# Kernel tuning notes

Hardware: AMD Instinct MI355X
Metric: run time of the kernel (lower is better)

## Reference

```python
import jax, jax.numpy as jnp
import numpy as np

FS = 64      # FIGURE_SEZE
HALF = 32    # FS // 2
STD = 12     # STD_LEN
BATCH = 4    # BATCH_SIZE
EPS = 1e-3   # keras BatchNormalization default epsilon
CC = 256     # cycleCount (multiple of BATCH)
D = FS * HALF  # 2048, dense in/out width


def _split(x):
    # Checkerboard boolean-mask gather: mask[i,j] = ((i + j) % 2 == 0).
    # Row-major flatten of data[mask] -> for even rows take even cols, odd rows odd cols.
    x4 = x.reshape(-1, FS, HALF, 2)                    # [N, FS, HALF, 2]
    par = (jnp.arange(FS) % 2)[None, :, None, None]    # per-row column parity
    u1 = jnp.take_along_axis(x4, par, axis=3)[..., 0]  # masked half   [N, FS, HALF]
    u2 = jnp.take_along_axis(x4, 1 - par, axis=3)[..., 0]  # demasked half
    return u1, u2


def _bn_dense(u, p):
    # computeF/computeG: flatten -> inference BatchNorm -> Dense(2048) -> reshape
    g, be, m, v, W, b = p
    s = u.reshape(u.shape[0], D)
    s = g * (s - m) * jax.lax.rsqrt(v + EPS) + be
    s = s @ W + b
    return s.reshape(-1, FS, HALF)


def _spread(w, off):
    # w @ expandM: place the 32 columns of w at columns off, off+2, ... of a 64-wide zero mat
    z = jnp.zeros((w.shape[0], FS, FS), w.dtype)
    return z.at[:, :, off::2].set(w)


def _move_even(mat, d):
    # keep even rows; roll odd rows along the column axis by d (== tf diag-matmul + roll)
    even = (jnp.arange(FS) % 2 == 0)[:, None]
    return jnp.where(even, mat, jnp.roll(mat, d, axis=2))


def _mix(w1, w2):
    return _move_even(_spread(w1, 0), -1) + _move_even(_spread(w2, 1), 1)


def _encoder(x, F, G):
    u1, u2 = _split(x.reshape(-1, FS, FS))
    v1 = u1 + _bn_dense(u2, F)
    w2 = u2 + _bn_dense(v1, G)
    return _mix(v1, w2).reshape(-1, STD, FS, FS)


def _decoder(y, F, G):
    w1, w2 = _split(y.reshape(-1, FS, FS))
    v2 = w2 - _bn_dense(w1, G)
    u1 = w1 - _bn_dense(v2, F)
    return _mix(u1, v2).reshape(-1, STD, FS, FS)


def _forward(inputs, W1, b1, g1, be1, m1, v1, W3, b3, g3, be3, m3, v3, kop):
    x = inputs                                   # [CC, STD, FS, FS]
    cc = x.shape[0]
    F = (g1, be1, m1, v1, W1, b1)
    G = (g3, be3, m3, v3, W3, b3)
    phiX = _encoder(x, F, G)
    dephiPhiX = _decoder(phiX, F, G)
    # Koopman step: reshape to [BATCH, cc//BATCH, ...], transpose, right-multiply K
    p = phiX.reshape(BATCH, cc // BATCH, STD, FS, FS).transpose(1, 0, 2, 3, 4)
    kPhix = (p @ kop).reshape(-1, STD, FS, FS)
    dePhiKPhiX = _decoder(kPhix, F, G)
    return (x, phiX, dephiPhiX, kPhix, dePhiKPhiX, x[:, 1:], phiX[:, 1:])


def setup_inputs() -> dict:
    key = jax.random.key(0)
    ks = jax.random.split(key, 16)
    inp = {
        "inputs": jax.random.normal(ks[0], (CC, STD, FS, FS), jnp.float32),
        "indexs": jax.random.randint(ks[1], (CC,), 0, 100),  # unused by forward
        "W1": jax.random.normal(ks[2], (D, 2048), jnp.float32) * 0.02,
        "b1": jnp.zeros((2048,), jnp.float32),
        "g1": jax.random.uniform(ks[3], (D,), jnp.float32, 0.9, 1.1),
        "be1": jax.random.normal(ks[4], (D,), jnp.float32) * 0.01,
        "m1": jax.random.normal(ks[5], (D,), jnp.float32) * 0.01,
        "v1": jax.random.uniform(ks[6], (D,), jnp.float32, 0.5, 1.5),
        "W3": jax.random.normal(ks[7], (D, 2048), jnp.float32) * 0.02,
        "b3": jnp.zeros((2048,), jnp.float32),
        "g3": jax.random.uniform(ks[8], (D,), jnp.float32, 0.9, 1.1),
        "be3": jax.random.normal(ks[9], (D,), jnp.float32) * 0.01,
        "m3": jax.random.normal(ks[10], (D,), jnp.float32) * 0.01,
        "v3": jax.random.uniform(ks[11], (D,), jnp.float32, 0.5, 1.5),
        "kop": jax.random.normal(ks[12], (FS, FS), jnp.float32) * 0.125,
    }
    return inp


def reference(inputs, indexs, W1, b1, g1, be1, m1, v1, W3, b3, g3, be3, m3, v3, kop):
    del indexs  # unused in the original call()
    return _forward(inputs, W1, b1, g1, be1, m1, v1, W3, b3, g3, be3, m3, v3, kop)
```

## Files before the change

### kernel.cpp

```cpp
#include <hip/hip_runtime.h>

#define DDIM 2048
#define NROWS 3072

typedef float f32x4 __attribute__((ext_vector_type(4)));
typedef __bf16 bf16x8 __attribute__((ext_vector_type(8)));

__device__ __forceinline__ unsigned short f32_bf16(float f) {
    unsigned int u = __float_as_uint(f);
    u += 0x7fffu + ((u >> 16) & 1u);
    return (unsigned short)(u >> 16);
}

__device__ __forceinline__ void gl2lds16(const unsigned short* g, unsigned short* l) {
    __builtin_amdgcn_global_load_lds(
        (__attribute__((address_space(1))) void*)g,
        (__attribute__((address_space(3))) void*)l, 16, 0, 0);
}

__global__ __launch_bounds__(256) void prep_scal(
    const float* __restrict__ g1, const float* __restrict__ be1,
    const float* __restrict__ m1, const float* __restrict__ v1,
    const float* __restrict__ b1, float* __restrict__ a1, float* __restrict__ c1, float* __restrict__ bp1,
    const float* __restrict__ g3, const float* __restrict__ be3,
    const float* __restrict__ m3, const float* __restrict__ v3,
    const float* __restrict__ b3, float* __restrict__ a3, float* __restrict__ c3, float* __restrict__ bp3)
{
    int n = blockIdx.x * 256 + threadIdx.x;
    if (n < DDIM) {
        float av1 = g1[n] / sqrtf(v1[n] + 1e-3f);
        a1[n] = av1; c1[n] = be1[n] - m1[n] * av1; bp1[n] = b1[n];
        float av3 = g3[n] / sqrtf(v3[n] + 1e-3f);
        a3[n] = av3; c3[n] = be3[n] - m3[n] * av3; bp3[n] = b3[n];
    }
}

__global__ __launch_bounds__(256) void prep_w(
    const float* __restrict__ W, const float* __restrict__ a, unsigned short* __restrict__ Wt)
{
    __shared__ float tile[64][65];
    const int kt = blockIdx.x * 64, nt = blockIdx.y * 64;
    const int t = threadIdx.x;
#pragma unroll
    for (int q = 0; q < 16; ++q) {
        int lin = q * 256 + t;
        int r = lin >> 6, c = lin & 63;
        tile[r][c] = a[kt + r] * W[(size_t)(kt + r) * DDIM + nt + c];
    }
    __syncthreads();
#pragma unroll
    for (int q = 0; q < 16; ++q) {
        int lin = q * 256 + t;
        int r = lin >> 6, c = lin & 63;
        Wt[(size_t)(nt + r) * DDIM + kt + c] = f32_bf16(tile[c][r]);
    }
}

__global__ __launch_bounds__(256) void prep_bpart(
    const float* __restrict__ W, const float* __restrict__ c, float* __restrict__ bp)
{
    int n = blockIdx.x * 256 + threadIdx.x;
    int k0 = blockIdx.y * 128;
    float acc = 0.f;
#pragma unroll 4
    for (int k = k0; k < k0 + 128; ++k) acc += c[k] * W[(size_t)k * DDIM + n];
    atomicAdd(&bp[n], acc);
}

__global__ __launch_bounds__(256) void split_x(
    const float* __restrict__ x, float* __restrict__ o0,
    float* __restrict__ o5, unsigned short* __restrict__ u2b)
{
    int idx = blockIdx.x * 256 + threadIdx.x;
    int n = idx >> 11, rem = idx & 2047, i = rem >> 5, h = rem & 31;
    int base = (n << 12) + (i << 6) + (h << 1);
    float2 xv = *(const float2*)(x + base);
    *(float2*)(o0 + base) = xv;
    int cc = n / 12, s = n - cc * 12;
    if (s >= 1) {
        int tb = ((cc * 11 + (s - 1)) << 12) + (i << 6) + (h << 1);
        *(float2*)(o5 + tb) = xv;
    }
    u2b[idx] = f32_bf16((i & 1) ? xv.x : xv.y);
}

template<bool TAIL>
__global__ __launch_bounds__(256) void mix_k(
    const float* __restrict__ A, const float* __restrict__ B,
    float* __restrict__ Y, float* __restrict__ Yt, unsigned short* __restrict__ Wb)
{
    int idx = blockIdx.x * 256 + threadIdx.x;
    int n = idx >> 11, rem = idx & 2047, i = rem >> 5, h = rem & 31;
    const float* Ar = A + (n << 11) + (i << 5);
    const float* Br = B + (n << 11) + (i << 5);
    float2 yv;
    if ((i & 1) == 0) { yv.x = Ar[h]; yv.y = Br[h]; }
    else             { yv.x = Br[(h + 31) & 31]; yv.y = Ar[(h + 1) & 31]; }
    int base = (n << 12) + (i << 6) + (h << 1);
    *(float2*)(Y + base) = yv;
    if (TAIL) {
        int cc = n / 12, s = n - cc * 12;
        if (s >= 1)
            *(float2*)(Yt + (((cc * 11 + s - 1) << 12) + (i << 6) + (h << 1))) = yv;
        Wb[idx] = f32_bf16((i & 1) ? yv.y : yv.x);
    }
}

__global__ __launch_bounds__(256) void koop_k(
    const float* __restrict__ phiX, const float* __restrict__ kop,
    float* __restrict__ out, unsigned short* __restrict__ Wb)
{
    __shared__ float P[64][65];
    __shared__ alignas(16) float Kp[64][64];
    const int t = threadIdx.x;
    const int np = blockIdx.x;
    int ccp = np / 12, s = np - ccp * 12;
    int src = (((ccp & 3) << 6) + (ccp >> 2)) * 12 + s;
    const float* Ps = phiX + (size_t)src * 4096;
#pragma unroll
    for (int q = 0; q < 16; ++q) {
        int lin = q * 256 + t, r = lin >> 6, c = lin & 63;
        P[r][c] = Ps[lin];
        Kp[r][c] = kop[lin];
    }
    __syncthreads();
    const int jq = (t & 15) << 2;
    const int i0 = (t >> 4) << 2;
    f32x4 acc[4];
#pragma unroll
    for (int r = 0; r < 4; ++r) acc[r] = f32x4{0.f, 0.f, 0.f, 0.f};
    for (int k = 0; k < 64; ++k) {
        f32x4 kv = *(const f32x4*)&Kp[k][jq];
#pragma unroll
        for (int r = 0; r < 4; ++r) acc[r] += P[i0 + r][k] * kv;
    }
    float* o = out + (size_t)np * 4096;
#pragma unroll
    for (int r = 0; r < 4; ++r) {
        const int i = i0 + r;
        *(f32x4*)(o + i * 64 + jq) = acc[r];
        const int par = i & 1;
        unsigned int w0 = f32_bf16(acc[r][par]);
        unsigned int w1v = f32_bf16(acc[r][2 + par]);
        *(unsigned int*)(Wb + (size_t)np * 2048 + i * 32 + (jq >> 1)) = w0 | (w1v << 16);
    }
}

template<int PARX, bool NEG, bool WBF>
__global__ __launch_bounds__(256, 3) void gemm_k(
    const unsigned short* __restrict__ Abf, const unsigned short* __restrict__ Wt,
    const float* __restrict__ bp, const float* __restrict__ resid,
    float* __restrict__ Cf, unsigned short* __restrict__ Cb)
{
    __shared__ alignas(16) unsigned short As[128][64];
    __shared__ alignas(16) unsigned short Bs[128][64];
    const int t = threadIdx.x;
    const int lane = t & 63, wave = t >> 6;
    const int quad = lane >> 4, l16 = lane & 15;
    const int m0 = blockIdx.x * 128;
    const int n0 = blockIdx.y * 128;
    const int wm = (wave >> 1) << 6;
    const int wn = (wave & 1) << 6;

    const int srow = lane >> 3;
    const int cdata = (lane & 7) ^ srow;
    const unsigned short* Ag = Abf + (size_t)(m0 + wave * 32 + srow) * DDIM + (cdata << 3);
    const unsigned short* Bg = Wt  + (size_t)(n0 + wave * 32 + srow) * DDIM + (cdata << 3);
    unsigned short* AslBase = &As[wave * 32][0];
    unsigned short* BslBase = &Bs[wave * 32][0];

    f32x4 acc[4][4];
#pragma unroll
    for (int a = 0; a < 4; ++a)
#pragma unroll
        for (int b = 0; b < 4; ++b) acc[a][b] = f32x4{0.f, 0.f, 0.f, 0.f};

    for (int k0 = 0; k0 < DDIM; k0 += 64) {
        __syncthreads();
#pragma unroll
        for (int j = 0; j < 4; ++j) {
            gl2lds16(Ag + (size_t)(j * 8) * DDIM + k0, AslBase + j * 8 * 64);
            gl2lds16(Bg + (size_t)(j * 8) * DDIM + k0, BslBase + j * 8 * 64);
        }
        __syncthreads();

#pragma unroll
        for (int kk = 0; kk < 2; ++kk) {
            bf16x8 af[4], bfr[4];
#pragma unroll
            for (int mi = 0; mi < 4; ++mi) {
                const int r = wm + mi * 16 + l16;
                af[mi] = *(const bf16x8*)&As[r][(((kk << 2) | quad) ^ (l16 & 7)) << 3];
            }
#pragma unroll
            for (int ni = 0; ni < 4; ++ni) {
                const int r = wn + ni * 16 + l16;
                bfr[ni] = *(const bf16x8*)&Bs[r][(((kk << 2) | quad) ^ (l16 & 7)) << 3];
            }
#pragma unroll
            for (int mi = 0; mi < 4; ++mi)
#pragma unroll
                for (int ni = 0; ni < 4; ++ni)
                    acc[mi][ni] = __builtin_amdgcn_mfma_f32_16x16x32_bf16(
                        af[mi], bfr[ni], acc[mi][ni], 0, 0, 0);
        }
    }

#pragma unroll
    for (int ni = 0; ni < 4; ++ni) {
        const int n = n0 + wn + ni * 16 + l16;
        const float bias = bp[n];
        const int i = n >> 5, h = n & 31;
        const int par = (i & 1) ^ PARX;
#pragma unroll
        for (int mi = 0; mi < 4; ++mi) {
            const int mbase = m0 + wm + mi * 16 + (quad << 2);
#pragma unroll
            for (int r = 0; r < 4; ++r) {
                const int mm = mbase + r;
                float cv = acc[mi][ni][r] + bias;
                float rs = resid[(size_t)(mm << 12) + (i << 6) + (h << 1) + par];
                float o = NEG ? (rs - cv) : (rs + cv);
                Cf[(size_t)mm * DDIM + n] = o;
                if constexpr (WBF) Cb[(size_t)mm * DDIM + n] = f32_bf16(o);
            }
        }
    }
}

extern "C" void kernel_launch(void* const* d_in, const int* in_sizes, int n_in,
                              void* d_out, int out_size, void* d_ws, size_t ws_size,
                              hipStream_t stream)
{
    (void)in_sizes; (void)n_in; (void)out_size; (void)ws_size;
    const float* x   = (const float*)d_in[0];
    const float* W1  = (const float*)d_in[2];
    const float* b1  = (const float*)d_in[3];
    const float* g1  = (const float*)d_in[4];
    const float* be1 = (const float*)d_in[5];
    const float* m1  = (const float*)d_in[6];
    const float* v1i = (const float*)d_in[7];
    const float* W3  = (const float*)d_in[8];
    const float* b3  = (const float*)d_in[9];
    const float* g3  = (const float*)d_in[10];
    const float* be3 = (const float*)d_in[11];
    const float* m3  = (const float*)d_in[12];
    const float* v3i = (const float*)d_in[13];
    const float* kop = (const float*)d_in[14];

    float* out = (float*)d_out;
    float* o0 = out;
    float* o1 = out + 12582912;
    float* o2 = out + 25165824;
    float* o3 = out + 37748736;
    float* o4 = out + 50331648;
    float* o5 = out + 62914560;
    float* o6 = out + 74448896;

    char* ws = (char*)d_ws;
    float* a1  = (float*)(ws);
    float* c1  = (float*)(ws + 8192);
    float* a3  = (float*)(ws + 16384);
    float* c3  = (float*)(ws + 24576);
    float* bp1 = (float*)(ws + 32768);
    float* bp3 = (float*)(ws + 40960);
    unsigned short* Wt1 = (unsigned short*)(ws + 49152);
    unsigned short* Wt3 = (unsigned short*)(ws + 49152 + 8388608);
    unsigned short* Abf = (unsigned short*)(ws + 49152 + 2u*8388608);
    unsigned short* Mbf = (unsigned short*)(ws + 49152 + 2u*8388608 + 12582912);
    float* Fa = (float*)(ws + 49152 + 2u*8388608 + 2u*12582912);
    float* Fb = (float*)(ws + 49152 + 2u*8388608 + 2u*12582912 + 25165824);

    prep_scal<<<8, 256, 0, stream>>>(g1, be1, m1, v1i, b1, a1, c1, bp1,
                                     g3, be3, m3, v3i, b3, a3, c3, bp3);
    prep_w<<<dim3(32, 32), 256, 0, stream>>>(W1, a1, Wt1);
    prep_w<<<dim3(32, 32), 256, 0, stream>>>(W3, a3, Wt3);
    prep_bpart<<<dim3(8, 16), 256, 0, stream>>>(W1, c1, bp1);
    prep_bpart<<<dim3(8, 16), 256, 0, stream>>>(W3, c3, bp3);
    split_x<<<24576, 256, 0, stream>>>(x, o0, o5, Abf);

    const dim3 gg(24, 16);
    gemm_k<0, false, true ><<<gg, 256, 0, stream>>>(Abf, Wt1, bp1, x, Fa, Mbf);
    gemm_k<1, false, false><<<gg, 256, 0, stream>>>(Mbf, Wt3, bp3, x, Fb, nullptr);
    mix_k<true><<<24576, 256, 0, stream>>>(Fa, Fb, o1, o6, Abf);

    gemm_k<1, true, true ><<<gg, 256, 0, stream>>>(Abf, Wt3, bp3, o1, Fa, Mbf);
    gemm_k<0, true, false><<<gg, 256, 0, stream>>>(Mbf, Wt1, bp1, o1, Fb, nullptr);
    mix_k<false><<<24576, 256, 0, stream>>>(Fb, Fa, o2, nullptr, nullptr);

    koop_k<<<3072, 256, 0, stream>>>(o1, kop, o3, Abf);

    gemm_k<1, true, true ><<<gg, 256, 0, stream>>>(Abf, Wt3, bp3, o3, Fa, Mbf);
    gemm_k<0, true, false><<<gg, 256, 0, stream>>>(Mbf, Wt1, bp1, o3, Fb, nullptr);
    mix_k<false><<<24576, 256, 0, stream>>>(Fb, Fa, o4, nullptr, nullptr);
}
```

Before: 818.8 us.

## Fuse mix into GEMM epilogues and batch both decoder passes into one GEMM

The interleaving mix kernels are removed. Their gather and roll logic, plus the output-tail copies, now run in the epilogue of the second GEMM of each encoder/decoder pair, which reads the first GEMM's float result as a partner. The encoder's first GEMM also writes a shifted bf16 copy that serves directly as the decoder input, so that split step is skipped. The two decoder passes (on phiX and on the Koopman output) are stacked into single M=6144 GEMM launches. Smaller changes fold the bias-correction reduction into prep_w and vectorise split_x. The aim is to cut several full-tensor memory round trips and kernel launches, in exchange for more complex epilogues with scattered partner reads and aliased workspace buffers.

After: 874.2 us. +6.8%, slower.

```diff
diff --git a/kernel.cpp b/kernel.cpp
--- a/kernel.cpp
+++ b/kernel.cpp
@@ -36,35 +36,34 @@
 }
 
 __global__ __launch_bounds__(256) void prep_w(
-    const float* __restrict__ W, const float* __restrict__ a, unsigned short* __restrict__ Wt)
+    const float* __restrict__ W, const float* __restrict__ a, const float* __restrict__ c,
+    unsigned short* __restrict__ Wt, float* __restrict__ bp)
 {
     __shared__ float tile[64][65];
+    __shared__ float red[4][64];
     const int kt = blockIdx.x * 64, nt = blockIdx.y * 64;
     const int t = threadIdx.x;
+    float part = 0.f;
 #pragma unroll
     for (int q = 0; q < 16; ++q) {
         int lin = q * 256 + t;
-        int r = lin >> 6, c = lin & 63;
-        tile[r][c] = a[kt + r] * W[(size_t)(kt + r) * DDIM + nt + c];
-    }
+        int r = lin >> 6, cl = lin & 63;
+        float w = W[(size_t)(kt + r) * DDIM + nt + cl];
+        tile[r][cl] = a[kt + r] * w;
+        part += c[kt + r] * w;
+    }
+    red[t >> 6][t & 63] = part;
     __syncthreads();
+    if (t < 64) {
+        float s = red[0][t] + red[1][t] + red[2][t] + red[3][t];
+        atomicAdd(&bp[nt + t], s);
+    }
 #pragma unroll
     for (int q = 0; q < 16; ++q) {
         int lin = q * 256 + t;
-        int r = lin >> 6, c = lin & 63;
-        Wt[(size_t)(nt + r) * DDIM + kt + c] = f32_bf16(tile[c][r]);
-    }
-}
-
-__global__ __launch_bounds__(256) void prep_bpart(
-    const float* __restrict__ W, const float* __restrict__ c, float* __restrict__ bp)
-{
-    int n = blockIdx.x * 256 + threadIdx.x;
-    int k0 = blockIdx.y * 128;
-    float acc = 0.f;
-#pragma unroll 4
-    for (int k = k0; k < k0 + 128; ++k) acc += c[k] * W[(size_t)k * DDIM + n];
-    atomicAdd(&bp[n], acc);
+        int r = lin >> 6, cl = lin & 63;
+        Wt[(size_t)(nt + r) * DDIM + kt + cl] = f32_bf16(tile[cl][r]);
+    }
 }
 
 __global__ __launch_bounds__(256) void split_x(
@@ -72,38 +71,19 @@
     float* __restrict__ o5, unsigned short* __restrict__ u2b)
 {
     int idx = blockIdx.x * 256 + threadIdx.x;
-    int n = idx >> 11, rem = idx & 2047, i = rem >> 5, h = rem & 31;
-    int base = (n << 12) + (i << 6) + (h << 1);
-    float2 xv = *(const float2*)(x + base);
-    *(float2*)(o0 + base) = xv;
+    int n = idx >> 10, rem = idx & 1023, i = rem >> 4, h2 = rem & 15;
+    int base = (n << 12) + (i << 6) + (h2 << 2);
+    f32x4 xv = *(const f32x4*)(x + base);
+    *(f32x4*)(o0 + base) = xv;
     int cc = n / 12, s = n - cc * 12;
     if (s >= 1) {
-        int tb = ((cc * 11 + (s - 1)) << 12) + (i << 6) + (h << 1);
-        *(float2*)(o5 + tb) = xv;
-    }
-    u2b[idx] = f32_bf16((i & 1) ? xv.x : xv.y);
-}
-
-template<bool TAIL>
-__global__ __launch_bounds__(256) void mix_k(
-    const float* __restrict__ A, const float* __restrict__ B,
-    float* __restrict__ Y, float* __restrict__ Yt, unsigned short* __restrict__ Wb)
-{
-    int idx = blockIdx.x * 256 + threadIdx.x;
-    int n = idx >> 11, rem = idx & 2047, i = rem >> 5, h = rem & 31;
-    const float* Ar = A + (n << 11) + (i << 5);
-    const float* Br = B + (n << 11) + (i << 5);
-    float2 yv;
-    if ((i & 1) == 0) { yv.x = Ar[h]; yv.y = Br[h]; }
-    else             { yv.x = Br[(h + 31) & 31]; yv.y = Ar[(h + 1) & 31]; }
-    int base = (n << 12) + (i << 6) + (h << 1);
-    *(float2*)(Y + base) = yv;
-    if (TAIL) {
-        int cc = n / 12, s = n - cc * 12;
-        if (s >= 1)
-            *(float2*)(Yt + (((cc * 11 + s - 1) << 12) + (i << 6) + (h << 1))) = yv;
-        Wb[idx] = f32_bf16((i & 1) ? yv.y : yv.x);
-    }
+        int tb = ((cc * 11 + (s - 1)) << 12) + (i << 6) + (h2 << 2);
+        *(f32x4*)(o5 + tb) = xv;
+    }
+    unsigned int w0, w1;
+    if ((i & 1) == 0) { w0 = f32_bf16(xv[1]); w1 = f32_bf16(xv[3]); }
+    else             { w0 = f32_bf16(xv[0]); w1 = f32_bf16(xv[2]); }
+    *(unsigned int*)(u2b + (size_t)n * DDIM + (i << 5) + (h2 << 1)) = w0 | (w1 << 16);
 }
 
 __global__ __launch_bounds__(256) void koop_k(
@@ -146,12 +126,18 @@
     }
 }
 
-template<int PARX, bool NEG, bool WBF>
+template<int MODE>
 __global__ __launch_bounds__(256, 3) void gemm_k(
     const unsigned short* __restrict__ Abf, const unsigned short* __restrict__ Wt,
-    const float* __restrict__ bp, const float* __restrict__ resid,
-    float* __restrict__ Cf, unsigned short* __restrict__ Cb)
-{
+    const float* __restrict__ bp, const float* __restrict__ resid0, const float* __restrict__ resid1,
+    float* __restrict__ out0, float* __restrict__ out1,
+    unsigned short* __restrict__ cb0, unsigned short* __restrict__ cb1,
+    const float* __restrict__ partner)
+{
+    constexpr int PARX = (MODE == 1 || MODE == 2) ? 1 : 0;
+    constexpr bool NEG  = (MODE >= 2);
+    constexpr bool DUAL = (MODE >= 2);
+
     __shared__ alignas(16) unsigned short As[128][64];
     __shared__ alignas(16) unsigned short Bs[128][64];
     const int t = threadIdx.x;
@@ -206,6 +192,8 @@
         }
     }
 
+    const bool second = DUAL && (m0 >= NROWS);
+
 #pragma unroll
     for (int ni = 0; ni < 4; ++ni) {
         const int n = n0 + wn + ni * 16 + l16;
@@ -218,11 +206,50 @@
 #pragma unroll
             for (int r = 0; r < 4; ++r) {
                 const int mm = mbase + r;
+                const int mloc = second ? (mm - NROWS) : mm;
                 float cv = acc[mi][ni][r] + bias;
-                float rs = resid[(size_t)(mm << 12) + (i << 6) + (h << 1) + par];
+                const float* rrow = (DUAL ? (second ? resid1 : resid0) : resid0)
+                                    + ((size_t)(DUAL ? mloc : mm) << 12);
+                float rs = rrow[(i << 6) + (h << 1) + par];
                 float o = NEG ? (rs - cv) : (rs + cv);
-                Cf[(size_t)mm * DDIM + n] = o;
-                if constexpr (WBF) Cb[(size_t)mm * DDIM + n] = f32_bf16(o);
+                if constexpr (MODE == 0) {
+                    out0[(size_t)mm * DDIM + n] = o;
+                    unsigned short us = f32_bf16(o);
+                    cb0[(size_t)mm * DDIM + n] = us;
+                    const int hw = (h - (i & 1)) & 31;
+                    cb1[(size_t)mm * DDIM + (i << 5) + hw] = us;
+                } else if constexpr (MODE == 2) {
+                    out0[(size_t)mm * DDIM + n] = o;
+                    cb0[(size_t)mm * DDIM + n] = f32_bf16(o);
+                } else if constexpr (MODE == 1) {
+                    float2 f2; int col;
+                    if ((i & 1) == 0) {
+                        col = h << 1;
+                        f2.x = partner[(size_t)mm * DDIM + n];
+                        f2.y = o;
+                    } else {
+                        col = ((h + 1) & 31) << 1;
+                        f2.x = o;
+                        f2.y = partner[(size_t)mm * DDIM + (i << 5) + ((h + 2) & 31)];
+                    }
+                    *(float2*)(out0 + ((size_t)mm << 12) + (i << 6) + col) = f2;
+                    int cc = mm / 12, s = mm - cc * 12;
+                    if (s >= 1)
+                        *(float2*)(out1 + ((size_t)(cc * 11 + s - 1) << 12) + (i << 6) + col) = f2;
+                } else {
+                    float2 f2; int col;
+                    if ((i & 1) == 0) {
+                        col = h << 1;
+                        f2.x = o;
+                        f2.y = partner[(size_t)mm * DDIM + n];
+                    } else {
+                        col = ((h + 31) & 31) << 1;
+                        f2.x = partner[(size_t)mm * DDIM + (i << 5) + ((h + 30) & 31)];
+                        f2.y = o;
+                    }
+                    float* yb = second ? out1 : out0;
+                    *(float2*)(yb + ((size_t)mloc << 12) + (i << 6) + col) = f2;
+                }
             }
         }
     }
@@ -265,32 +292,29 @@
     float* bp1 = (float*)(ws + 32768);
     float* bp3 = (float*)(ws + 40960);
     unsigned short* Wt1 = (unsigned short*)(ws + 49152);
-    unsigned short* Wt3 = (unsigned short*)(ws + 49152 + 8388608);
-    unsigned short* Abf = (unsigned short*)(ws + 49152 + 2u*8388608);
-    unsigned short* Mbf = (unsigned short*)(ws + 49152 + 2u*8388608 + 12582912);
-    float* Fa = (float*)(ws + 49152 + 2u*8388608 + 2u*12582912);
-    float* Fb = (float*)(ws + 49152 + 2u*8388608 + 2u*12582912 + 25165824);
+    unsigned short* Wt3 = (unsigned short*)(ws + 8437760);
+    unsigned short* Abf = (unsigned short*)(ws + 16826368);
+    unsigned short* Mbf = (unsigned short*)(ws + 29409280);
+    unsigned short* Dbf = (unsigned short*)(ws + 41992192);
+    unsigned short* Kbf = (unsigned short*)(ws + 54575104);
+    float* Fa  = (float*)(ws + 67158016);
+    float* Ga  = (float*)(ws + 67158016);
+    unsigned short* Gbf = (unsigned short*)(ws + 16826368);
 
     prep_scal<<<8, 256, 0, stream>>>(g1, be1, m1, v1i, b1, a1, c1, bp1,
                                      g3, be3, m3, v3i, b3, a3, c3, bp3);
-    prep_w<<<dim3(32, 32), 256, 0, stream>>>(W1, a1, Wt1);
-    prep_w<<<dim3(32, 32), 256, 0, stream>>>(W3, a3, Wt3);
-    prep_bpart<<<dim3(8, 16), 256, 0, stream>>>(W1, c1, bp1);
-    prep_bpart<<<dim3(8, 16), 256, 0, stream>>>(W3, c3, bp3);
-    split_x<<<24576, 256, 0, stream>>>(x, o0, o5, Abf);
-
-    const dim3 gg(24, 16);
-    gemm_k<0, false, true ><<<gg, 256, 0, stream>>>(Abf, Wt1, bp1, x, Fa, Mbf);
-    gemm_k<1, false, false><<<gg, 256, 0, stream>>>(Mbf, Wt3, bp3, x, Fb, nullptr);
-    mix_k<true><<<24576, 256, 0, stream>>>(Fa, Fb, o1, o6, Abf);
-
-    gemm_k<1, true, true ><<<gg, 256, 0, stream>>>(Abf, Wt3, bp3, o1, Fa, Mbf);
-    gemm_k<0, true, false><<<gg, 256, 0, stream>>>(Mbf, Wt1, bp1, o1, Fb, nullptr);
-    mix_k<false><<<24576, 256, 0, stream>>>(Fb, Fa, o2, nullptr, nullptr);
-
-    koop_k<<<3072, 256, 0, stream>>>(o1, kop, o3, Abf);
-
-    gemm_k<1, true, true ><<<gg, 256, 0, stream>>>(Abf, Wt3, bp3, o3, Fa, Mbf);
-    gemm_k<0, true, false><<<gg, 256, 0, stream>>>(Mbf, Wt1, bp1, o3, Fb, nullptr);
-    mix_k<false><<<24576, 256, 0, stream>>>(Fb, Fa, o4, nullptr, nullptr);
-}
+    prep_w<<<dim3(32, 32), 256, 0, stream>>>(W1, a1, c1, Wt1, bp1);
+    prep_w<<<dim3(32, 32), 256, 0, stream>>>(W3, a3, c3, Wt3, bp3);
+    split_x<<<12288, 256, 0, stream>>>(x, o0, o5, Abf);
+
+    const dim3 ge(24, 16);
+    const dim3 gd(48, 16);
+
+    gemm_k<0><<<ge, 256, 0, stream>>>(Abf, Wt1, bp1, x, nullptr, Fa, nullptr, Mbf, Dbf, nullptr);
+    gemm_k<1><<<ge, 256, 0, stream>>>(Mbf, Wt3, bp3, x, nullptr, o1, o6, nullptr, nullptr, Fa);
+
+    koop_k<<<3072, 256, 0, stream>>>(o1, kop, o3, Kbf);
+
+    gemm_k<2><<<gd, 256, 0, stream>>>(Dbf, Wt3, bp3, o1, o3, Ga, nullptr, Gbf, nullptr, nullptr);
+    gemm_k<3><<<gd, 256, 0, stream>>>(Gbf, Wt1, bp1, o1, o3, o2, o4, nullptr, nullptr, Ga);
+}
```
